# Kernel tuning notes

Measured on AMD Instinct MI355X. Metric: run time of the kernel, lower is better.

The kernel has to match this reference:

```python
import jax, jax.numpy as jnp
import numpy as np

B, N, F, D, H, S_OBJ, S_REG, ITERS = 32, 1024, 1152, 512, 8, 8, 4, 3
S = S_OBJ + S_REG
HD = D // H
SCALE = HD ** -0.5


def ln(x, g, b, eps=1e-5):
    m = x.mean(-1, keepdims=True)
    v = ((x - m) ** 2).mean(-1, keepdims=True)
    return (x - m) / jnp.sqrt(v + eps) * g + b


def setup_inputs() -> dict:
    key = jax.random.key(0)
    ks = jax.random.split(key, 16)
    s = 0.02
    d = {
        'features': jax.random.normal(ks[0], (B, N, F), jnp.float32),
        'noise': jax.random.normal(ks[1], (B, S, D), jnp.float32),
        'w_in': jax.random.normal(ks[2], (F, D), jnp.float32) * s,
        'b_in': jnp.zeros((D,), jnp.float32),
        'ln1_g': jnp.ones((D,), jnp.float32), 'ln1_b': jnp.zeros((D,), jnp.float32),
        'slot_mu': jax.random.normal(ks[3], (1, S, D), jnp.float32) * D ** -0.5,
        'slot_log_sigma': jnp.zeros((1, S, D), jnp.float32),
        'wq': jax.random.normal(ks[4], (D, D), jnp.float32) * s,
        'wk': jax.random.normal(ks[5], (D, D), jnp.float32) * s,
        'wv': jax.random.normal(ks[6], (D, D), jnp.float32) * s,
        'gru_wih': jax.random.normal(ks[7], (D, 3 * D), jnp.float32) * s,
        'gru_whh': jax.random.normal(ks[8], (D, 3 * D), jnp.float32) * s,
        'gru_bih': jnp.zeros((3 * D,), jnp.float32),
        'gru_bhh': jnp.zeros((3 * D,), jnp.float32),
        'nslots_g': jnp.ones((D,), jnp.float32), 'nslots_b': jnp.zeros((D,), jnp.float32),
        'ninput_g': jnp.ones((D,), jnp.float32), 'ninput_b': jnp.zeros((D,), jnp.float32),
        'ffn_ln_g': jnp.ones((D,), jnp.float32), 'ffn_ln_b': jnp.zeros((D,), jnp.float32),
        'ffn_w1': jax.random.normal(ks[9], (D, 4 * D), jnp.float32) * s,
        'ffn_b1': jnp.zeros((4 * D,), jnp.float32),
        'ffn_w2': jax.random.normal(ks[10], (4 * D, D), jnp.float32) * s,
        'ffn_b2': jnp.zeros((D,), jnp.float32),
        'sel_w1': jax.random.normal(ks[11], (D, D // 2), jnp.float32) * s,
        'sel_b1': jnp.zeros((D // 2,), jnp.float32),
        'sel_w2': jax.random.normal(ks[12], (D // 2, 2), jnp.float32) * s,
        'sel_b2': jnp.zeros((2,), jnp.float32),
    }
    return d


def reference(features, noise, w_in, b_in, ln1_g, ln1_b, slot_mu, slot_log_sigma,
              wq, wk, wv, gru_wih, gru_whh, gru_bih, gru_bhh,
              nslots_g, nslots_b, ninput_g, ninput_b,
              ffn_ln_g, ffn_ln_b, ffn_w1, ffn_b1, ffn_w2, ffn_b2,
              sel_w1, sel_b1, sel_w2, sel_b2):
    b = features.shape[0]
    # input_proj: Linear + LayerNorm, then norm_input LayerNorm
    x = ln(features @ w_in + b_in, ln1_g, ln1_b)
    inp = ln(x, ninput_g, ninput_b)
    slots = slot_mu + jnp.exp(slot_log_sigma) * noise  # [B,S,D]
    k = (inp @ wk).reshape(b, N, H, HD)
    v = (inp @ wv).reshape(b, N, H, HD)
    attn_out = None
    for _ in range(ITERS):
        sn = ln(slots, nslots_g, nslots_b)
        q = (sn @ wq).reshape(b, S, H, HD)
        dots = jnp.einsum('bihd,bjhd->bihj', q, k) * SCALE  # [B,S,H,N]
        # softmax over flattened (slot, head) axis per key j
        attn = jax.nn.softmax(dots.reshape(b, S * H, N), axis=1).reshape(b, S, H, N)
        attn_out = attn.mean(axis=2)  # [B,S,N]
        attn_n = (attn + 1e-8) / (attn.sum(axis=-1, keepdims=True) + 1e-8)
        upd = jnp.einsum('bjhd,bihj->bihd', v, attn_n).reshape(b * S, D)
        h = slots.reshape(b * S, D)
        gx = upd @ gru_wih + gru_bih
        gh = h @ gru_whh + gru_bhh
        xr, xz, xn = jnp.split(gx, 3, axis=-1)
        hr, hz, hn = jnp.split(gh, 3, axis=-1)
        r = jax.nn.sigmoid(xr + hr)
        z = jax.nn.sigmoid(xz + hz)
        n = jnp.tanh(xn + r * hn)
        slots = ((1.0 - z) * n + z * h).reshape(b, S, D)
        f = ln(slots, ffn_ln_g, ffn_ln_b)
        f = jax.nn.gelu(f @ ffn_w1 + ffn_b1, approximate=False) @ ffn_w2 + ffn_b2
        slots = slots + f
    obj = slots[:, :S_OBJ]  # [B,num_slots,D]
    logits = jax.nn.relu(obj @ sel_w1 + sel_b1) @ sel_w2 + sel_b2  # [B,num_slots,2]
    decision = (jnp.argmax(logits, axis=-1) == 1).astype(slots.dtype)
    # eval-mode repair: ensure >=2 active slots per row (deterministic: first inactive)
    needed = jnp.maximum(0.0, 2.0 - decision.sum(-1, keepdims=True))
    inactive_rank = jnp.cumsum(1.0 - decision, axis=-1)
    add = ((decision == 0) & (inactive_rank <= needed)).astype(decision.dtype)
    decision = decision + add
    obj = obj * decision[..., None]
    return obj, decision, attn_out[:, :S_OBJ]
```

## Files before the change

### kernel.cpp

```cpp
#include <hip/hip_runtime.h>
#include <math.h>

typedef __attribute__((ext_vector_type(8))) short short8;
typedef __attribute__((ext_vector_type(4))) float f32x4;

typedef const __attribute__((address_space(1))) void gv_t;
typedef __attribute__((address_space(3))) void lv_t;

__device__ __forceinline__ float b2f(short u) {
  union { unsigned int i; float f; } c; c.i = ((unsigned int)(unsigned short)u) << 16; return c.f;
}
__device__ __forceinline__ short f2b(float f) {
  union { float f; unsigned int i; } c; c.f = f;
  unsigned int r = c.i + 0x7FFFu + ((c.i >> 16) & 1u);
  return (short)(r >> 16);
}
__device__ __forceinline__ void glds(const short* g, short* l) {
  __builtin_amdgcn_global_load_lds((gv_t*)g, (lv_t*)l, 16, 0, 0);
}


__global__ __launch_bounds__(256) void k_convA(const float* __restrict__ in, short* __restrict__ out, int n8) {
  int idx = blockIdx.x * 256 + threadIdx.x;
  if (idx >= n8) return;
  const float4* p = (const float4*)(in + (size_t)idx * 8);
  float4 a = p[0], b = p[1];
  short8 r;
  r[0]=f2b(a.x); r[1]=f2b(a.y); r[2]=f2b(a.z); r[3]=f2b(a.w);
  r[4]=f2b(b.x); r[5]=f2b(b.y); r[6]=f2b(b.z); r[7]=f2b(b.w);
  *(short8*)(out + (size_t)idx*8) = r;
}


__global__ __launch_bounds__(256) void k_prep(
    const float* __restrict__ w_in, const float* __restrict__ wk, const float* __restrict__ wv,
    const float* __restrict__ wq, const float* __restrict__ wih, const float* __restrict__ whh,
    const float* __restrict__ bih, const float* __restrict__ bhh,
    const float* __restrict__ w1, const float* __restrict__ w2, const float* __restrict__ sl1,
    const float* __restrict__ mu, const float* __restrict__ lsig, const float* __restrict__ noise,
    short* __restrict__ Bt1, short* __restrict__ Btkv, short* __restrict__ wq_t,
    short* __restrict__ wgru, float* __restrict__ gbias,
    short* __restrict__ w1_t, short* __restrict__ w2_t, short* __restrict__ sl1_t,
    float* __restrict__ slots, short* __restrict__ gruA)
{
  int blk = blockIdx.x, t = threadIdx.x;
  if (blk < 2304) {
    int idx = blk*256 + t;
    int kk = idx / 512, n = idx % 512;
    Bt1[(size_t)n*1152 + kk] = f2b(w_in[idx]);
  } else if (blk < 4352) {
    int idx = (blk-2304)*256 + t;
    int kk = idx >> 10, n = idx & 1023;
    float v = (n < 512) ? wk[kk*512 + n] : wv[kk*512 + (n-512)];
    Btkv[(size_t)n*512 + kk] = f2b(v);
  } else if (blk < 5376) {
    int idx = (blk-4352)*256 + t;
    int kk = idx >> 9, n = idx & 511;
    wq_t[n*512 + kk] = f2b(wq[idx]);
  } else if (blk < 13568) {
    int idx = (blk-5376)*256 + t;
    int n = idx >> 10, k = idx & 1023;
    int g = n >> 9, c = n & 511;
    float v;
    if (g == 0)      v = (k < 512) ? wih[k*1536 + c]        : whh[(k-512)*1536 + c];
    else if (g == 1) v = (k < 512) ? wih[k*1536 + 512 + c]  : whh[(k-512)*1536 + 512 + c];
    else if (g == 2) v = (k < 512) ? wih[k*1536 + 1024 + c] : 0.f;
    else             v = (k < 512) ? 0.f                    : whh[(k-512)*1536 + 1024 + c];
    wgru[(size_t)n*1024 + k] = f2b(v);
  } else if (blk < 17664) {
    int idx = (blk-13568)*256 + t;
    int kk = idx >> 11, n = idx & 2047;
    w1_t[(size_t)n*512 + kk] = f2b(w1[idx]);
  } else if (blk < 21760) {
    int idx = (blk-17664)*256 + t;
    int kk = idx >> 9, n = idx & 511;
    w2_t[(size_t)n*2048 + kk] = f2b(w2[idx]);
  } else if (blk < 22272) {
    int idx = (blk-21760)*256 + t;
    int kk = idx >> 8, n = idx & 255;
    sl1_t[n*512 + kk] = f2b(sl1[idx]);
  } else if (blk < 22280) {
    int n = (blk-22272)*256 + t;
    int g = n >> 9;
    float v;
    if (g <= 1)      v = bih[n] + bhh[n];
    else if (g == 2) v = bih[n];
    else             v = bhh[1024 + (n - 1536)];
    gbias[n] = v;
  } else {
    int idx = (blk-22280)*256 + t;
    int sd = idx % 6144;
    float v = mu[sd] + __expf(lsig[sd]) * noise[idx];
    slots[idx] = v;
    int row = idx >> 9, c = idx & 511;
    gruA[(size_t)row*1024 + 512 + c] = f2b(v);
  }
}


__global__ __launch_bounds__(256) void gemm_p(
    const short* __restrict__ A, const short* __restrict__ Bt,
    const float* __restrict__ bias, short* __restrict__ Cb,
    int N, int K, int lda, int ldb)
{
  __shared__ short As[2][128*64];
  __shared__ short Bs[2][128*64];
  const int t = threadIdx.x;
  const int lane = t & 63, wave = t >> 6;

  const int nwg = gridDim.x, gridX = N >> 7, orig = blockIdx.x;
  const int q = nwg >> 3, r = nwg & 7, xcd = orig & 7, base = orig >> 3;
  const int wgid = (xcd < r ? xcd*(q+1) : r*(q+1) + (xcd - r)*q) + base;
  const int bx = wgid % gridX, by = wgid / gridX;

  const int rowBase = by * 128, colBase = bx * 128;
  const int wm = (wave >> 1) * 64, wn = (wave & 1) * 64;
  const int fr = lane & 15, kcf = lane >> 4;
  f32x4 acc[4][4] = {};

  int srow[4], scol[4];
  #pragma unroll
  for (int i = 0; i < 4; ++i) {
    int c = i*256 + t;
    srow[i] = c >> 3;
    scol[i] = ((c & 7) ^ (srow[i] & 7)) * 8;
  }

  const int nsteps = K >> 6;
  auto STAGE = [&](int step, int buf) {
    int kb = step * 64;
    #pragma unroll
    for (int i = 0; i < 4; ++i) {
      int c = i*256 + t;
      glds(A + (size_t)(rowBase + srow[i])*lda + kb + scol[i], As[buf] + c*8);
      glds(Bt + (size_t)(colBase + srow[i])*ldb + kb + scol[i], Bs[buf] + c*8);
    }
  };

  STAGE(0, 0);
  if (nsteps > 1) { STAGE(1, 1); asm volatile("s_waitcnt vmcnt(8)" ::: "memory"); }
  else            {              asm volatile("s_waitcnt vmcnt(0)" ::: "memory"); }
  __builtin_amdgcn_sched_barrier(0);
  __builtin_amdgcn_s_barrier();
  __builtin_amdgcn_sched_barrier(0);

  for (int tt = 0; tt < nsteps; ++tt) {
    const int cur = tt & 1;
    short8 af[2][4], bf[2][4];
    #pragma unroll
    for (int ks = 0; ks < 2; ++ks) {
      int kc = ks*4 + kcf;
      #pragma unroll
      for (int m = 0; m < 4; ++m) {
        int rowa = wm + m*16 + fr;
        af[ks][m] = *(const short8*)(As[cur] + rowa*64 + (kc ^ (rowa & 7))*8);
        int rowb = wn + m*16 + fr;
        bf[ks][m] = *(const short8*)(Bs[cur] + rowb*64 + (kc ^ (rowb & 7))*8);
      }
    }
    asm volatile("s_waitcnt lgkmcnt(0)" ::: "memory");
    __builtin_amdgcn_sched_barrier(0);
    __builtin_amdgcn_s_barrier();
    __builtin_amdgcn_sched_barrier(0);
    if (tt + 2 < nsteps) STAGE(tt + 2, cur);
    #pragma unroll
    for (int ks = 0; ks < 2; ++ks)
      #pragma unroll
      for (int m = 0; m < 4; ++m)
        #pragma unroll
        for (int n = 0; n < 4; ++n)
          acc[m][n] = __builtin_amdgcn_mfma_f32_16x16x32_bf16(af[ks][m], bf[ks][n], acc[m][n], 0, 0, 0);
    if (tt + 1 < nsteps) {
      if (tt + 2 < nsteps) asm volatile("s_waitcnt vmcnt(8)" ::: "memory");
      else                 asm volatile("s_waitcnt vmcnt(0)" ::: "memory");
      __builtin_amdgcn_sched_barrier(0);
      __builtin_amdgcn_s_barrier();
      __builtin_amdgcn_sched_barrier(0);
    }
  }

  const int cr = (lane >> 4) * 4, cc2 = lane & 15;
  #pragma unroll
  for (int m = 0; m < 4; ++m)
    #pragma unroll
    for (int n = 0; n < 4; ++n) {
      int col = colBase + wn + n*16 + cc2;
      float bv = bias ? bias[col] : 0.f;
      #pragma unroll
      for (int j = 0; j < 4; ++j) {
        int row = rowBase + wm + m*16 + cr + j;
        Cb[(size_t)row*N + col] = f2b(acc[m][n][j] + bv);
      }
    }
}


template<int ACT, bool OUTBF, bool SPLITK>
__global__ __launch_bounds__(256) void gemm_t(
    const short* __restrict__ A, const short* __restrict__ Bt,
    const float* __restrict__ bias,
    float* __restrict__ Cf, short* __restrict__ Cb,
    int N, int Kp, int lda, int ldb, int ldf, int ldcb, int cboff, int skstride)
{
  __shared__ short As[128*64];
  __shared__ short Bs[128*64];
  const int t = threadIdx.x;
  const int lane = t & 63, wave = t >> 6;

  const int nwg = gridDim.x, gridX = N >> 7, orig = blockIdx.x;
  const int q = nwg >> 3, r = nwg & 7, xcd = orig & 7, base = orig >> 3;
  const int wgid = (xcd < r ? xcd*(q+1) : r*(q+1) + (xcd - r)*q) + base;
  const int bx = wgid % gridX, by = wgid / gridX;

  const int rowBase = by * 128, colBase = bx * 128;
  const size_t koff = (size_t)blockIdx.y * Kp;
  const int wm = (wave >> 1) * 64, wn = (wave & 1) * 64;
  const int fr = lane & 15, kcf = lane >> 4;
  f32x4 acc[4][4] = {};

  int srow[4], scol[4];
  #pragma unroll
  for (int i = 0; i < 4; ++i) {
    int c = i*256 + t;
    srow[i] = c >> 3;
    scol[i] = ((c & 7) ^ (srow[i] & 7)) * 8;
  }

  for (int kb = 0; kb < Kp; kb += 64) {
    __syncthreads();
    #pragma unroll
    for (int i = 0; i < 4; ++i) {
      int c = i*256 + t;
      glds(A + (size_t)(rowBase + srow[i])*lda + koff + kb + scol[i], As + c*8);
      glds(Bt + (size_t)(colBase + srow[i])*ldb + koff + kb + scol[i], Bs + c*8);
    }
    __syncthreads();
    #pragma unroll
    for (int ks = 0; ks < 2; ++ks) {
      short8 af[4], bf[4];
      #pragma unroll
      for (int m = 0; m < 4; ++m) {
        int row = wm + m*16 + fr;
        int kc = ks*4 + kcf;
        af[m] = *(const short8*)(As + row*64 + (kc ^ (row & 7))*8);
      }
      #pragma unroll
      for (int n = 0; n < 4; ++n) {
        int row = wn + n*16 + fr;
        int kc = ks*4 + kcf;
        bf[n] = *(const short8*)(Bs + row*64 + (kc ^ (row & 7))*8);
      }
      #pragma unroll
      for (int m = 0; m < 4; ++m)
        #pragma unroll
        for (int n = 0; n < 4; ++n)
          acc[m][n] = __builtin_amdgcn_mfma_f32_16x16x32_bf16(af[m], bf[n], acc[m][n], 0, 0, 0);
    }
  }

  const int cr = (lane >> 4) * 4, cc2 = lane & 15;
  if (SPLITK) {
    float* dst = Cf + (size_t)blockIdx.y * skstride;
    #pragma unroll
    for (int m = 0; m < 4; ++m)
      #pragma unroll
      for (int n = 0; n < 4; ++n) {
        int col = colBase + wn + n*16 + cc2;
        #pragma unroll
        for (int j = 0; j < 4; ++j) {
          int row = rowBase + wm + m*16 + cr + j;
          dst[(size_t)row * ldf + col] = acc[m][n][j];
        }
      }
  } else {
    #pragma unroll
    for (int m = 0; m < 4; ++m)
      #pragma unroll
      for (int n = 0; n < 4; ++n) {
        int col = colBase + wn + n*16 + cc2;
        float bv = bias ? bias[col] : 0.f;
        #pragma unroll
        for (int j = 0; j < 4; ++j) {
          int row = rowBase + wm + m*16 + cr + j;
          float v = acc[m][n][j] + bv;
          if (ACT == 1) v = 0.5f*v*(1.f + erff(v*0.70710678118f));
          else if (ACT == 2) v = fmaxf(v, 0.f);
          if (OUTBF) Cb[(size_t)row*ldcb + cboff + col] = f2b(v);
          else Cf[(size_t)row*ldf + col] = v;
        }
      }
  }
}


__global__ __launch_bounds__(256) void k_gruact_sk(const float* __restrict__ p, const float* __restrict__ gbias,
                                                   float* __restrict__ slots)
{
  int idx = blockIdx.x*256 + threadIdx.x;
  int row = idx >> 9, c = idx & 511;
  const float* base = p + (size_t)row*2048 + c;
  float g0=gbias[c], g1=gbias[512+c], g2=gbias[1024+c], g3=gbias[1536+c];
  #pragma unroll
  for (int s = 0; s < 4; ++s) {
    const float* qq = base + (size_t)s*786432;
    g0 += qq[0]; g1 += qq[512]; g2 += qq[1024]; g3 += qq[1536];
  }
  float r = 1.f/(1.f+__expf(-g0));
  float z = 1.f/(1.f+__expf(-g1));
  float n = tanhf(g2 + r*g3);
  slots[idx] = (1.f-z)*n + z*slots[idx];
}

__global__ __launch_bounds__(256) void k_ffn1red(const float* __restrict__ p, const float* __restrict__ b1,
                                                 short* __restrict__ f1) {
  int i = blockIdx.x*256 + threadIdx.x;
  int col = (i*8) & 2047;
  float v[8], w[8];
  *(float4*)v = *(const float4*)(p + (size_t)i*8);
  *(float4*)(v+4) = *(const float4*)(p + (size_t)i*8 + 4);
  const float* p2 = p + 786432;
  *(float4*)w = *(const float4*)(p2 + (size_t)i*8);
  *(float4*)(w+4) = *(const float4*)(p2 + (size_t)i*8 + 4);
  short8 o;
  #pragma unroll
  for (int e = 0; e < 8; ++e) {
    float x = v[e] + w[e] + b1[col + e];
    x = 0.5f*x*(1.f + erff(x*0.70710678118f));
    o[e] = f2b(x);
  }
  *(short8*)(f1 + (size_t)i*8) = o;
}

__global__ __launch_bounds__(256) void k_ffn2red(const float* __restrict__ p, const float* __restrict__ b2,
                                                 float* __restrict__ slots, short* __restrict__ gruA) {
  int i = blockIdx.x*256 + threadIdx.x;
  int base = i*8;
  int row = base >> 9, c = base & 511;
  float v[8] = {0.f,0.f,0.f,0.f,0.f,0.f,0.f,0.f};
  #pragma unroll
  for (int s = 0; s < 8; ++s) {
    const float* qq = p + (size_t)s*196608 + base;
    float4 a = *(const float4*)qq, b = *(const float4*)(qq+4);
    v[0]+=a.x; v[1]+=a.y; v[2]+=a.z; v[3]+=a.w;
    v[4]+=b.x; v[5]+=b.y; v[6]+=b.z; v[7]+=b.w;
  }
  float sl[8];
  *(float4*)sl = *(const float4*)(slots + base);
  *(float4*)(sl+4) = *(const float4*)(slots + base + 4);
  short8 o;
  #pragma unroll
  for (int e = 0; e < 8; ++e) {
    float ns = sl[e] + v[e] + b2[c+e];
    sl[e] = ns;
    o[e] = f2b(ns);
  }
  *(float4*)(slots + base) = *(float4*)sl;
  *(float4*)(slots + base + 4) = *(float4*)(sl+4);
  *(short8*)(gruA + (size_t)row*1024 + 512 + c) = o;
}


__global__ __launch_bounds__(256) void k_ln2(const short* __restrict__ y, short* __restrict__ inp,
    const float* __restrict__ g1, const float* __restrict__ b1,
    const float* __restrict__ g2, const float* __restrict__ b2)
{
  int t = threadIdx.x, lane = t & 63;
  int row = blockIdx.x * 4 + (t >> 6);
  const short8 raw = *(const short8*)(y + (size_t)row*512 + lane*8);
  float x[8];
  #pragma unroll
  for (int e = 0; e < 8; ++e) x[e] = b2f(raw[e]);
  float s = 0.f, ss = 0.f;
  #pragma unroll
  for (int e = 0; e < 8; ++e) { s += x[e]; ss += x[e]*x[e]; }
  #pragma unroll
  for (int m = 1; m < 64; m <<= 1) { s += __shfl_xor(s, m, 64); ss += __shfl_xor(ss, m, 64); }
  float mean = s * (1.f/512.f);
  float rs = rsqrtf(ss*(1.f/512.f) - mean*mean + 1e-5f);
  int c = lane * 8;
  #pragma unroll
  for (int e = 0; e < 8; ++e) x[e] = (x[e]-mean)*rs*g1[c+e] + b1[c+e];
  s = 0.f; ss = 0.f;
  #pragma unroll
  for (int e = 0; e < 8; ++e) { s += x[e]; ss += x[e]*x[e]; }
  #pragma unroll
  for (int m = 1; m < 64; m <<= 1) { s += __shfl_xor(s, m, 64); ss += __shfl_xor(ss, m, 64); }
  float mean2 = s * (1.f/512.f);
  float rs2 = rsqrtf(ss*(1.f/512.f) - mean2*mean2 + 1e-5f);
  short8 o;
  #pragma unroll
  for (int e = 0; e < 8; ++e) o[e] = f2b((x[e]-mean2)*rs2*g2[c+e] + b2[c+e]);
  *(short8*)(inp + (size_t)row*512 + lane*8) = o;
}


__global__ __launch_bounds__(256) void k_lnb(const float* __restrict__ x, short* __restrict__ out,
    const float* __restrict__ g, const float* __restrict__ b)
{
  int t = threadIdx.x, lane = t & 63;
  int row = blockIdx.x * 4 + (t >> 6);
  const float* src = x + (size_t)row*512 + lane*8;
  float v[8];
  *(float4*)v = *(const float4*)src;
  *(float4*)(v+4) = *(const float4*)(src+4);
  float s = 0.f, ss = 0.f;
  #pragma unroll
  for (int e = 0; e < 8; ++e) { s += v[e]; ss += v[e]*v[e]; }
  #pragma unroll
  for (int m = 1; m < 64; m <<= 1) { s += __shfl_xor(s, m, 64); ss += __shfl_xor(ss, m, 64); }
  float mean = s * (1.f/512.f);
  float rs = rsqrtf(ss*(1.f/512.f) - mean*mean + 1e-5f);
  int c = lane * 8;
  short8 o;
  #pragma unroll
  for (int e = 0; e < 8; ++e) o[e] = f2b((v[e]-mean)*rs*g[c+e] + b[c+e]);
  *(short8*)(out + (size_t)row*512 + c) = o;
}


__global__ __launch_bounds__(256) void k_attn(
    const float* __restrict__ qparts, const short* __restrict__ kv,
    float* __restrict__ pvp, float* __restrict__ denp, float* __restrict__ aout)
{
  __shared__ float qs[12][512];
  __shared__ float ksh[128][65];
  __shared__ float dots[96][132];
  const int t = threadIdx.x;
  const int jt = blockIdx.x, b = blockIdx.y;

  for (int i = t; i < 6144; i += 256) {
    int s = i >> 9, d = i & 511;
    size_t o = (size_t)(b*12+s)*512 + d;
    qs[s][d] = qparts[o] + qparts[196608 + o] + qparts[393216 + o] + qparts[589824 + o];
  }

  const int jj = t & 127, sg = t >> 7;
  for (int h = 0; h < 8; ++h) {
    __syncthreads();
    #pragma unroll
    for (int i = 0; i < 4; ++i) {
      int c = i*256 + t;
      int j2 = c >> 3, seg = (c & 7) * 8;
      short8 raw = *(const short8*)(kv + ((size_t)(b*1024 + jt*128 + j2))*1024 + h*64 + seg);
      #pragma unroll
      for (int e = 0; e < 8; ++e) ksh[j2][seg+e] = b2f(raw[e]);
    }
    __syncthreads();
    float d6[6] = {};
    for (int d = 0; d < 64; ++d) {
      float kvv = ksh[jj][d];
      #pragma unroll
      for (int i = 0; i < 6; ++i) d6[i] += qs[sg*6+i][h*64+d] * kvv;
    }
    #pragma unroll
    for (int i = 0; i < 6; ++i) dots[(sg*6+i)*8 + h][jj] = d6[i] * 0.125f;
  }
  __syncthreads();

  {
    int j = t >> 1, half = (t & 1) * 48;
    float mx = -1e30f;
    #pragma unroll
    for (int i = 0; i < 48; ++i) mx = fmaxf(mx, dots[half+i][j]);
    mx = fmaxf(mx, __shfl_xor(mx, 1, 64));
    float ex[48];
    float sum = 0.f;
    #pragma unroll
    for (int i = 0; i < 48; ++i) { ex[i] = __expf(dots[half+i][j] - mx); sum += ex[i]; }
    sum += __shfl_xor(sum, 1, 64);
    float inv = 1.f / sum;
    float as_[6] = {0,0,0,0,0,0};
    #pragma unroll
    for (int i = 0; i < 48; ++i) {
      float a = ex[i] * inv;
      dots[half+i][j] = a;
      as_[i >> 3] += a;
    }
    if (aout) {
      int sbase = (t & 1) * 6;
      #pragma unroll
      for (int q2 = 0; q2 < 6; ++q2) {
        int s = sbase + q2;
        if (s < 8) aout[((size_t)(b*8+s))*1024 + jt*128 + j] = as_[q2] * 0.125f;
      }
    }
  }

  const int d = t & 63, sq = t >> 6;
  for (int h = 0; h < 8; ++h) {
    __syncthreads();
    #pragma unroll
    for (int i = 0; i < 4; ++i) {
      int c = i*256 + t;
      int j2 = c >> 3, seg = (c & 7) * 8;
      short8 raw = *(const short8*)(kv + ((size_t)(b*1024 + jt*128 + j2))*1024 + 512 + h*64 + seg);
      #pragma unroll
      for (int e = 0; e < 8; ++e) ksh[j2][seg+e] = b2f(raw[e]);
    }
    __syncthreads();
    float a3[3] = {0.f, 0.f, 0.f};
    for (int j2 = 0; j2 < 128; ++j2) {
      float vv = ksh[j2][d];
      #pragma unroll
      for (int i = 0; i < 3; ++i) a3[i] += dots[(sq + 4*i)*8 + h][j2] * vv;
    }
    #pragma unroll
    for (int i = 0; i < 3; ++i)
      pvp[((size_t)(jt*32+b))*6144 + (sq + 4*i)*512 + h*64 + d] = a3[i];
    if (t < 12) {
      float ls = 0.f;
      for (int j2 = 0; j2 < 128; ++j2) ls += dots[t*8 + h][j2];
      denp[((size_t)(jt*32+b))*96 + t*8 + h] = ls;
    }
  }
}


__global__ __launch_bounds__(256) void k_pvred(const float* __restrict__ pvp, const float* __restrict__ denp,
                                               short* __restrict__ gruA)
{
  __shared__ float den[96];
  int t = threadIdx.x, b = blockIdx.x;
  if (t < 96) {
    float s = 0.f;
    #pragma unroll
    for (int jt2 = 0; jt2 < 8; ++jt2) s += denp[((size_t)(jt2*32+b))*96 + t];
    den[t] = s + 1e-8f;
  }
  __syncthreads();
  for (int i = t; i < 6144; i += 256) {
    int s = i >> 9, rem = i & 511, h = rem >> 6;
    float acc = 0.f;
    #pragma unroll
    for (int jt2 = 0; jt2 < 8; ++jt2) acc += pvp[((size_t)(jt2*32+b))*6144 + i];
    gruA[((size_t)(b*12+s))*1024 + rem] = f2b(acc / den[s*8 + h]);
  }
}


__global__ __launch_bounds__(64) void k_decide(const float* __restrict__ hid, const float* __restrict__ w2,
    const float* __restrict__ b2, const float* __restrict__ slots, float* __restrict__ out)
{
  __shared__ float lg[16];
  __shared__ float dec[8];
  int b = blockIdx.x, t = threadIdx.x;
  if (t < 16) {
    int s = t >> 1, cl = t & 1;
    const float* hr = hid + (size_t)(b*12+s)*256;
    float a = b2[cl];
    for (int k = 0; k < 256; ++k) a += hr[k] * w2[k*2+cl];
    lg[t] = a;
  }
  __syncthreads();
  if (t == 0) {
    float d0[8]; float tot = 0.f;
    #pragma unroll
    for (int s = 0; s < 8; ++s) { d0[s] = (lg[2*s+1] > lg[2*s]) ? 1.f : 0.f; tot += d0[s]; }
    float needed = fmaxf(0.f, 2.f - tot);
    float cum = 0.f;
    #pragma unroll
    for (int s = 0; s < 8; ++s) {
      cum += 1.f - d0[s];
      float add = (d0[s] == 0.f && cum <= needed) ? 1.f : 0.f;
      float dd = d0[s] + add;
      dec[s] = dd;
      out[131072 + b*8 + s] = dd;
    }
  }
  __syncthreads();
  for (int i = 0; i < 64; ++i) {
    int idx = i*64 + t;
    int s = idx >> 9, c = idx & 511;
    out[(size_t)(b*8+s)*512 + c] = slots[(size_t)(b*12+s)*512 + c] * dec[s];
  }
}


extern "C" void kernel_launch(void* const* d_in, const int* in_sizes, int n_in,
                              void* d_out, int out_size, void* d_ws, size_t ws_size,
                              hipStream_t stream) {
  const float* features = (const float*)d_in[0];
  const float* noise    = (const float*)d_in[1];
  const float* w_in     = (const float*)d_in[2];
  const float* b_in     = (const float*)d_in[3];
  const float* ln1_g    = (const float*)d_in[4];
  const float* ln1_b    = (const float*)d_in[5];
  const float* slot_mu  = (const float*)d_in[6];
  const float* slot_ls  = (const float*)d_in[7];
  const float* wq       = (const float*)d_in[8];
  const float* wk       = (const float*)d_in[9];
  const float* wv       = (const float*)d_in[10];
  const float* gru_wih  = (const float*)d_in[11];
  const float* gru_whh  = (const float*)d_in[12];
  const float* gru_bih  = (const float*)d_in[13];
  const float* gru_bhh  = (const float*)d_in[14];
  const float* nslots_g = (const float*)d_in[15];
  const float* nslots_b = (const float*)d_in[16];
  const float* ninput_g = (const float*)d_in[17];
  const float* ninput_b = (const float*)d_in[18];
  const float* ffnln_g  = (const float*)d_in[19];
  const float* ffnln_b  = (const float*)d_in[20];
  const float* ffn_w1   = (const float*)d_in[21];
  const float* ffn_b1   = (const float*)d_in[22];
  const float* ffn_w2   = (const float*)d_in[23];
  const float* ffn_b2   = (const float*)d_in[24];
  const float* sel_w1   = (const float*)d_in[25];
  const float* sel_b1   = (const float*)d_in[26];
  const float* sel_w2   = (const float*)d_in[27];
  const float* sel_b2   = (const float*)d_in[28];
  float* out = (float*)d_out;
  float* fnull = (float*)nullptr;
  short* snull = (short*)nullptr;

  char* w = (char*)d_ws;
  size_t off = 0;
  auto alloc = [&](size_t n) { char* p = w + off; off = (off + n + 255) & ~255ULL; return p; };
  short* Abf   = (short*)alloc(75497472);
  short* kv    = Abf;
  short* ybf   = (short*)alloc(33554432);
  short* inp   = (short*)alloc(33554432);
  short* Bt1   = (short*)alloc(1179648);
  short* Btkv  = (short*)alloc(1048576);
  short* wq_t  = (short*)alloc(524288);
  short* wgru  = (short*)alloc(4194304);
  float* gbias = (float*)alloc(8192);
  short* w1_t  = (short*)alloc(2097152);
  short* w2_t  = (short*)alloc(2097152);
  short* sl1_t = (short*)alloc(262144);
  float* slots = (float*)alloc(786432);
  short* gruA  = (short*)alloc(786432);
  short* sn    = (short*)alloc(393216);
  float* parts = (float*)alloc(12582912);
  float* pvp   = (float*)alloc(6291456);
  float* denp  = (float*)alloc(98304);
  short* fln   = (short*)alloc(393216);
  short* f1    = (short*)alloc(1572864);
  float* hid   = (float*)alloc(393216);
  (void)ws_size; (void)in_sizes; (void)n_in; (void)out_size;

  k_convA<<<dim3(18432), dim3(256), 0, stream>>>(features, Abf, 4718592);
  k_prep<<<dim3(23048), dim3(256), 0, stream>>>(
      w_in, wk, wv, wq, gru_wih, gru_whh, gru_bih, gru_bhh,
      ffn_w1, ffn_w2, sel_w1, slot_mu, slot_ls, noise,
      Bt1, Btkv, wq_t, wgru, gbias, w1_t, w2_t, sl1_t, slots, gruA);

  gemm_p<<<dim3(1024), dim3(256), 0, stream>>>(Abf, Bt1, b_in, ybf, 512, 1152, 1152, 1152);
  k_ln2<<<dim3(8192), dim3(256), 0, stream>>>(ybf, inp, ln1_g, ln1_b, ninput_g, ninput_b);
  gemm_p<<<dim3(2048), dim3(256), 0, stream>>>(inp, Btkv, fnull, kv, 1024, 512, 512, 512);

  for (int it = 0; it < 3; ++it) {
    k_lnb<<<dim3(96), dim3(256), 0, stream>>>(slots, sn, nslots_g, nslots_b);
    gemm_t<0,false,true><<<dim3(12, 4), dim3(256), 0, stream>>>(
        sn, wq_t, fnull, parts, snull, 512, 128, 512, 512, 512, 0, 0, 196608);
    k_attn<<<dim3(8, 32), dim3(256), 0, stream>>>(parts, kv, pvp, denp,
        it == 2 ? out + 131328 : fnull);
    k_pvred<<<dim3(32), dim3(256), 0, stream>>>(pvp, denp, gruA);
    gemm_t<0,false,true><<<dim3(48, 4), dim3(256), 0, stream>>>(
        gruA, wgru, fnull, parts, snull, 2048, 256, 1024, 1024, 2048, 0, 0, 786432);
    k_gruact_sk<<<dim3(768), dim3(256), 0, stream>>>(parts, gbias, slots);
    k_lnb<<<dim3(96), dim3(256), 0, stream>>>(slots, fln, ffnln_g, ffnln_b);
    gemm_t<0,false,true><<<dim3(48, 2), dim3(256), 0, stream>>>(
        fln, w1_t, fnull, parts, snull, 2048, 256, 512, 512, 2048, 0, 0, 786432);
    k_ffn1red<<<dim3(384), dim3(256), 0, stream>>>(parts, ffn_b1, f1);
    gemm_t<0,false,true><<<dim3(12, 8), dim3(256), 0, stream>>>(
        f1, w2_t, fnull, parts, snull, 512, 256, 2048, 2048, 512, 0, 0, 196608);
    k_ffn2red<<<dim3(96), dim3(256), 0, stream>>>(parts, ffn_b2, slots, gruA);
  }

  gemm_t<2,false,false><<<dim3(6), dim3(256), 0, stream>>>(
      gruA + 512, sl1_t, sel_b1, hid, snull, 256, 512, 1024, 512, 256, 0, 0, 0);
  k_decide<<<dim3(32), dim3(64), 0, stream>>>(hid, sel_w2, sel_b2, slots, out);
}
```

Baseline: 551.7 us.

## Fuse GRU/LN and FFN epilogues, merge feature conversion, prefetch K in attention

```diff
diff --git a/kernel.cpp b/kernel.cpp
--- a/kernel.cpp
+++ b/kernel.cpp
@@ -17,18 +17,6 @@
 }
 __device__ __forceinline__ void glds(const short* g, short* l) {
   __builtin_amdgcn_global_load_lds((gv_t*)g, (lv_t*)l, 16, 0, 0);
-}
-
-
-__global__ __launch_bounds__(256) void k_convA(const float* __restrict__ in, short* __restrict__ out, int n8) {
-  int idx = blockIdx.x * 256 + threadIdx.x;
-  if (idx >= n8) return;
-  const float4* p = (const float4*)(in + (size_t)idx * 8);
-  float4 a = p[0], b = p[1];
-  short8 r;
-  r[0]=f2b(a.x); r[1]=f2b(a.y); r[2]=f2b(a.z); r[3]=f2b(a.w);
-  r[4]=f2b(b.x); r[5]=f2b(b.y); r[6]=f2b(b.z); r[7]=f2b(b.w);
-  *(short8*)(out + (size_t)idx*8) = r;
 }
 
 
@@ -38,13 +26,22 @@
     const float* __restrict__ bih, const float* __restrict__ bhh,
     const float* __restrict__ w1, const float* __restrict__ w2, const float* __restrict__ sl1,
     const float* __restrict__ mu, const float* __restrict__ lsig, const float* __restrict__ noise,
+    const float* __restrict__ features,
     short* __restrict__ Bt1, short* __restrict__ Btkv, short* __restrict__ wq_t,
     short* __restrict__ wgru, float* __restrict__ gbias,
     short* __restrict__ w1_t, short* __restrict__ w2_t, short* __restrict__ sl1_t,
-    float* __restrict__ slots, short* __restrict__ gruA)
+    float* __restrict__ slots, short* __restrict__ gruA, short* __restrict__ Abf)
 {
   int blk = blockIdx.x, t = threadIdx.x;
-  if (blk < 2304) {
+  if (blk >= 23048) {
+    int idx = (blk-23048)*256 + t;
+    const float4* p = (const float4*)(features + (size_t)idx * 8);
+    float4 a = p[0], b = p[1];
+    short8 r;
+    r[0]=f2b(a.x); r[1]=f2b(a.y); r[2]=f2b(a.z); r[3]=f2b(a.w);
+    r[4]=f2b(b.x); r[5]=f2b(b.y); r[6]=f2b(b.z); r[7]=f2b(b.w);
+    *(short8*)(Abf + (size_t)idx*8) = r;
+  } else if (blk < 2304) {
     int idx = blk*256 + t;
     int kk = idx / 512, n = idx % 512;
     Bt1[(size_t)n*1152 + kk] = f2b(w_in[idx]);
@@ -293,70 +290,84 @@
 }
 
 
-__global__ __launch_bounds__(256) void k_gruact_sk(const float* __restrict__ p, const float* __restrict__ gbias,
-                                                   float* __restrict__ slots)
-{
-  int idx = blockIdx.x*256 + threadIdx.x;
-  int row = idx >> 9, c = idx & 511;
-  const float* base = p + (size_t)row*2048 + c;
-  float g0=gbias[c], g1=gbias[512+c], g2=gbias[1024+c], g3=gbias[1536+c];
-  #pragma unroll
-  for (int s = 0; s < 4; ++s) {
-    const float* qq = base + (size_t)s*786432;
-    g0 += qq[0]; g1 += qq[512]; g2 += qq[1024]; g3 += qq[1536];
-  }
-  float r = 1.f/(1.f+__expf(-g0));
-  float z = 1.f/(1.f+__expf(-g1));
-  float n = tanhf(g2 + r*g3);
-  slots[idx] = (1.f-z)*n + z*slots[idx];
-}
-
-__global__ __launch_bounds__(256) void k_ffn1red(const float* __restrict__ p, const float* __restrict__ b1,
-                                                 short* __restrict__ f1) {
-  int i = blockIdx.x*256 + threadIdx.x;
-  int col = (i*8) & 2047;
-  float v[8], w[8];
-  *(float4*)v = *(const float4*)(p + (size_t)i*8);
-  *(float4*)(v+4) = *(const float4*)(p + (size_t)i*8 + 4);
-  const float* p2 = p + 786432;
-  *(float4*)w = *(const float4*)(p2 + (size_t)i*8);
-  *(float4*)(w+4) = *(const float4*)(p2 + (size_t)i*8 + 4);
+__global__ __launch_bounds__(256) void k_gruln(const float* __restrict__ p, const float* __restrict__ gbias,
+    float* __restrict__ slots, short* __restrict__ fln,
+    const float* __restrict__ g, const float* __restrict__ bb)
+{
+  int t = threadIdx.x, lane = t & 63;
+  int row = blockIdx.x*4 + (t >> 6);
+  int c = lane * 8;
+  float hold[8], v[8];
+  *(float4*)hold     = *(const float4*)(slots + (size_t)row*512 + c);
+  *(float4*)(hold+4) = *(const float4*)(slots + (size_t)row*512 + c + 4);
+  const float* base = p + (size_t)row*2048;
+  #pragma unroll
+  for (int e = 0; e < 8; ++e) {
+    int cc = c + e;
+    float g0=gbias[cc], g1=gbias[512+cc], g2=gbias[1024+cc], g3=gbias[1536+cc];
+    #pragma unroll
+    for (int s = 0; s < 4; ++s) {
+      const float* qq = base + (size_t)s*786432 + cc;
+      g0 += qq[0]; g1 += qq[512]; g2 += qq[1024]; g3 += qq[1536];
+    }
+    float r = 1.f/(1.f+__expf(-g0));
+    float z = 1.f/(1.f+__expf(-g1));
+    float n = tanhf(g2 + r*g3);
+    v[e] = (1.f-z)*n + z*hold[e];
+  }
+  *(float4*)(slots + (size_t)row*512 + c)     = *(float4*)v;
+  *(float4*)(slots + (size_t)row*512 + c + 4) = *(float4*)(v+4);
+  float s1 = 0.f, s2 = 0.f;
+  #pragma unroll
+  for (int e = 0; e < 8; ++e) { s1 += v[e]; s2 += v[e]*v[e]; }
+  #pragma unroll
+  for (int m = 1; m < 64; m <<= 1) { s1 += __shfl_xor(s1, m, 64); s2 += __shfl_xor(s2, m, 64); }
+  float mean = s1 * (1.f/512.f);
+  float rs = rsqrtf(s2*(1.f/512.f) - mean*mean + 1e-5f);
   short8 o;
   #pragma unroll
-  for (int e = 0; e < 8; ++e) {
-    float x = v[e] + w[e] + b1[col + e];
-    x = 0.5f*x*(1.f + erff(x*0.70710678118f));
-    o[e] = f2b(x);
-  }
-  *(short8*)(f1 + (size_t)i*8) = o;
-}
-
-__global__ __launch_bounds__(256) void k_ffn2red(const float* __restrict__ p, const float* __restrict__ b2,
-                                                 float* __restrict__ slots, short* __restrict__ gruA) {
-  int i = blockIdx.x*256 + threadIdx.x;
-  int base = i*8;
-  int row = base >> 9, c = base & 511;
-  float v[8] = {0.f,0.f,0.f,0.f,0.f,0.f,0.f,0.f};
+  for (int e = 0; e < 8; ++e) o[e] = f2b((v[e]-mean)*rs*g[c+e] + bb[c+e]);
+  *(short8*)(fln + (size_t)row*512 + c) = o;
+}
+
+
+__global__ __launch_bounds__(256) void k_ffn2redln(const float* __restrict__ p, const float* __restrict__ b2,
+    float* __restrict__ slots, short* __restrict__ gruA, short* __restrict__ sn,
+    const float* __restrict__ g, const float* __restrict__ bb)
+{
+  int t = threadIdx.x, lane = t & 63;
+  int row = blockIdx.x*4 + (t >> 6);
+  int c = lane * 8;
+  size_t base = (size_t)row*512 + c;
+  float v[8];
+  *(float4*)v     = *(const float4*)(slots + base);
+  *(float4*)(v+4) = *(const float4*)(slots + base + 4);
+  #pragma unroll
+  for (int e = 0; e < 8; ++e) v[e] += b2[c+e];
   #pragma unroll
   for (int s = 0; s < 8; ++s) {
     const float* qq = p + (size_t)s*196608 + base;
-    float4 a = *(const float4*)qq, b = *(const float4*)(qq+4);
+    float4 a = *(const float4*)qq, b4 = *(const float4*)(qq+4);
     v[0]+=a.x; v[1]+=a.y; v[2]+=a.z; v[3]+=a.w;
-    v[4]+=b.x; v[5]+=b.y; v[6]+=b.z; v[7]+=b.w;
-  }
-  float sl[8];
-  *(float4*)sl = *(const float4*)(slots + base);
-  *(float4*)(sl+4) = *(const float4*)(slots + base + 4);
+    v[4]+=b4.x; v[5]+=b4.y; v[6]+=b4.z; v[7]+=b4.w;
+  }
+  *(float4*)(slots + base)     = *(float4*)v;
+  *(float4*)(slots + base + 4) = *(float4*)(v+4);
   short8 o;
   #pragma unroll
-  for (int e = 0; e < 8; ++e) {
-    float ns = sl[e] + v[e] + b2[c+e];
-    sl[e] = ns;
-    o[e] = f2b(ns);
-  }
-  *(float4*)(slots + base) = *(float4*)sl;
-  *(float4*)(slots + base + 4) = *(float4*)(sl+4);
+  for (int e = 0; e < 8; ++e) o[e] = f2b(v[e]);
   *(short8*)(gruA + (size_t)row*1024 + 512 + c) = o;
+  float s1 = 0.f, s2 = 0.f;
+  #pragma unroll
+  for (int e = 0; e < 8; ++e) { s1 += v[e]; s2 += v[e]*v[e]; }
+  #pragma unroll
+  for (int m = 1; m < 64; m <<= 1) { s1 += __shfl_xor(s1, m, 64); s2 += __shfl_xor(s2, m, 64); }
+  float mean = s1 * (1.f/512.f);
+  float rs = rsqrtf(s2*(1.f/512.f) - mean*mean + 1e-5f);
+  short8 o2;
+  #pragma unroll
+  for (int e = 0; e < 8; ++e) o2[e] = f2b((v[e]-mean)*rs*g[c+e] + bb[c+e]);
+  *(short8*)(sn + base) = o2;
 }
 
 
@@ -423,10 +434,19 @@
     float* __restrict__ pvp, float* __restrict__ denp, float* __restrict__ aout)
 {
   __shared__ float qs[12][512];
+  __shared__ short kbf[2][128*64];
   __shared__ float ksh[128][65];
   __shared__ float dots[96][132];
   const int t = threadIdx.x;
   const int jt = blockIdx.x, b = blockIdx.y;
+  const short* kvb = kv + ((size_t)(b*1024 + jt*128))*1024;
+
+  #pragma unroll
+  for (int i = 0; i < 4; ++i) {
+    int c = i*256 + t;
+    int j2 = c >> 3, d0 = c & 7;
+    glds(kvb + (size_t)j2*1024 + ((d0 ^ (j2 & 7))*8), kbf[0] + c*8);
+  }
 
   for (int i = t; i < 6144; i += 256) {
     int s = i >> 9, d = i & 511;
@@ -436,26 +456,34 @@
 
   const int jj = t & 127, sg = t >> 7;
   for (int h = 0; h < 8; ++h) {
+    if (h < 7) {
+      #pragma unroll
+      for (int i = 0; i < 4; ++i) {
+        int c = i*256 + t;
+        int j2 = c >> 3, d0 = c & 7;
+        glds(kvb + (size_t)j2*1024 + (h+1)*64 + ((d0 ^ (j2 & 7))*8), kbf[(h+1)&1] + c*8);
+      }
+      asm volatile("s_waitcnt vmcnt(4)" ::: "memory");
+    } else {
+      asm volatile("s_waitcnt vmcnt(0)" ::: "memory");
+    }
     __syncthreads();
-    #pragma unroll
-    for (int i = 0; i < 4; ++i) {
-      int c = i*256 + t;
-      int j2 = c >> 3, seg = (c & 7) * 8;
-      short8 raw = *(const short8*)(kv + ((size_t)(b*1024 + jt*128 + j2))*1024 + h*64 + seg);
-      #pragma unroll
-      for (int e = 0; e < 8; ++e) ksh[j2][seg+e] = b2f(raw[e]);
-    }
+    const short* kb = kbf[h & 1];
+    float d6[6] = {};
+    #pragma unroll
+    for (int g = 0; g < 8; ++g) {
+      short8 kk = *(const short8*)(kb + jj*64 + ((g ^ (jj & 7))*8));
+      #pragma unroll
+      for (int e = 0; e < 8; ++e) {
+        float kd = b2f(kk[e]);
+        #pragma unroll
+        for (int i = 0; i < 6; ++i) d6[i] += qs[sg*6+i][h*64 + g*8 + e] * kd;
+      }
+    }
+    #pragma unroll
+    for (int i = 0; i < 6; ++i) dots[(sg*6+i)*8 + h][jj] = d6[i] * 0.125f;
     __syncthreads();
-    float d6[6] = {};
-    for (int d = 0; d < 64; ++d) {
-      float kvv = ksh[jj][d];
-      #pragma unroll
-      for (int i = 0; i < 6; ++i) d6[i] += qs[sg*6+i][h*64+d] * kvv;
-    }
-    #pragma unroll
-    for (int i = 0; i < 6; ++i) dots[(sg*6+i)*8 + h][jj] = d6[i] * 0.125f;
-  }
-  __syncthreads();
+  }
 
   {
     int j = t >> 1, half = (t & 1) * 48;
@@ -493,7 +521,7 @@
     for (int i = 0; i < 4; ++i) {
       int c = i*256 + t;
       int j2 = c >> 3, seg = (c & 7) * 8;
-      short8 raw = *(const short8*)(kv + ((size_t)(b*1024 + jt*128 + j2))*1024 + 512 + h*64 + seg);
+      short8 raw = *(const short8*)(kvb + (size_t)j2*1024 + 512 + h*64 + seg);
       #pragma unroll
       for (int e = 0; e < 8; ++e) ksh[j2][seg+e] = b2f(raw[e]);
     }
@@ -638,18 +666,18 @@
   float* hid   = (float*)alloc(393216);
   (void)ws_size; (void)in_sizes; (void)n_in; (void)out_size;
 
-  k_convA<<<dim3(18432), dim3(256), 0, stream>>>(features, Abf, 4718592);
-  k_prep<<<dim3(23048), dim3(256), 0, stream>>>(
+  k_prep<<<dim3(41480), dim3(256), 0, stream>>>(
       w_in, wk, wv, wq, gru_wih, gru_whh, gru_bih, gru_bhh,
-      ffn_w1, ffn_w2, sel_w1, slot_mu, slot_ls, noise,
-      Bt1, Btkv, wq_t, wgru, gbias, w1_t, w2_t, sl1_t, slots, gruA);
+      ffn_w1, ffn_w2, sel_w1, slot_mu, slot_ls, noise, features,
+      Bt1, Btkv, wq_t, wgru, gbias, w1_t, w2_t, sl1_t, slots, gruA, Abf);
 
   gemm_p<<<dim3(1024), dim3(256), 0, stream>>>(Abf, Bt1, b_in, ybf, 512, 1152, 1152, 1152);
   k_ln2<<<dim3(8192), dim3(256), 0, stream>>>(ybf, inp, ln1_g, ln1_b, ninput_g, ninput_b);
   gemm_p<<<dim3(2048), dim3(256), 0, stream>>>(inp, Btkv, fnull, kv, 1024, 512, 512, 512);
 
+  k_lnb<<<dim3(96), dim3(256), 0, stream>>>(slots, sn, nslots_g, nslots_b);
+
   for (int it = 0; it < 3; ++it) {
-    k_lnb<<<dim3(96), dim3(256), 0, stream>>>(slots, sn, nslots_g, nslots_b);
     gemm_t<0,false,true><<<dim3(12, 4), dim3(256), 0, stream>>>(
         sn, wq_t, fnull, parts, snull, 512, 128, 512, 512, 512, 0, 0, 196608);
     k_attn<<<dim3(8, 32), dim3(256), 0, stream>>>(parts, kv, pvp, denp,
@@ -657,14 +685,13 @@
     k_pvred<<<dim3(32), dim3(256), 0, stream>>>(pvp, denp, gruA);
     gemm_t<0,false,true><<<dim3(48, 4), dim3(256), 0, stream>>>(
         gruA, wgru, fnull, parts, snull, 2048, 256, 1024, 1024, 2048, 0, 0, 786432);
-    k_gruact_sk<<<dim3(768), dim3(256), 0, stream>>>(parts, gbias, slots);
-    k_lnb<<<dim3(96), dim3(256), 0, stream>>>(slots, fln, ffnln_g, ffnln_b);
-    gemm_t<0,false,true><<<dim3(48, 2), dim3(256), 0, stream>>>(
-        fln, w1_t, fnull, parts, snull, 2048, 256, 512, 512, 2048, 0, 0, 786432);
-    k_ffn1red<<<dim3(384), dim3(256), 0, stream>>>(parts, ffn_b1, f1);
+    k_gruln<<<dim3(96), dim3(256), 0, stream>>>(parts, gbias, slots, fln, ffnln_g, ffnln_b);
+    gemm_t<1,true,false><<<dim3(48), dim3(256), 0, stream>>>(
+        fln, w1_t, ffn_b1, fnull, f1, 2048, 512, 512, 512, 2048, 2048, 0, 0);
     gemm_t<0,false,true><<<dim3(12, 8), dim3(256), 0, stream>>>(
         f1, w2_t, fnull, parts, snull, 512, 256, 2048, 2048, 512, 0, 0, 196608);
-    k_ffn2red<<<dim3(96), dim3(256), 0, stream>>>(parts, ffn_b2, slots, gruA);
+    k_ffn2redln<<<dim3(96), dim3(256), 0, stream>>>(parts, ffn_b2, slots, gruA, sn,
+        nslots_g, nslots_b);
   }
 
   gemm_t<2,false,false><<<dim3(6), dim3(256), 0, stream>>>(
```

After: 625.3 us. +13.4%, slower.
